# Kernel optimization log

Hardware: AMD Instinct MI355X
Metric: run time of the kernel (lower is better)

## Reference

```python
import jax, jax.numpy as jnp
import numpy as np


def _safe_div(w, n):
    # tf.math.divide_no_nan: returns 0 where denominator is 0
    n = n[:, None]
    return jnp.where(n > 0, w / jnp.where(n > 0, n, 1.0), 0.0)


def setup_inputs() -> dict:
    key = jax.random.key(0)
    x = jax.random.normal(key, (16, 32768, 256), dtype=jnp.float32)
    return {"x": x}


def reference(x):
    # x: [n_models, n_samples, dim]
    n_models = x.shape[0]
    xt = jnp.transpose(x, (1, 0, 2))  # [ns, nm, dim]
    v0 = xt[:, 0, :]
    basis_list = [_safe_div(v0, jnp.linalg.norm(v0, axis=1))]  # each [ns, dim]
    for i in range(1, n_models):
        B = jnp.stack(basis_list, axis=1)              # [ns, i, dim]
        v = xt[:, i, :]                                # [ns, dim]
        coef = jnp.einsum('nd,nid->ni', v, B)          # projections onto basis
        w = v - jnp.einsum('ni,nid->nd', coef, B)      # classical Gram-Schmidt step
        basis_list.append(_safe_div(w, jnp.linalg.norm(w, axis=1)))
    return jnp.stack(basis_list, axis=0)               # [n_models, ns, dim]
```

## Files before the change

kernel.cpp:

```cpp
#include <hip/hip_runtime.h>


constexpr int NM = 16;
constexpr int NR = 32768;
constexpr int D4 = 64;

template <int CTRL, int RMASK>
__device__ __forceinline__ float dpp_add(float x) {
    int xi = __builtin_bit_cast(int, x);
    int yi = __builtin_amdgcn_update_dpp(0, xi, CTRL, RMASK, 0xF, false);
    return x + __builtin_bit_cast(float, yi);
}

__device__ __forceinline__ float wave_sum64(float x) {
    x = dpp_add<0xB1,  0xF>(x);
    x = dpp_add<0x4E,  0xF>(x);
    x = dpp_add<0x141, 0xF>(x);
    x = dpp_add<0x140, 0xF>(x);
    x = dpp_add<0x142, 0xA>(x);
    x = dpp_add<0x143, 0xC>(x);
    int s = __builtin_amdgcn_readlane(__builtin_bit_cast(int, x), 63);
    return __builtin_bit_cast(float, s);
}

__device__ __forceinline__ float dot4(const float4& a, const float4& b) {
    return a.x * b.x + a.y * b.y + a.z * b.z + a.w * b.w;
}

__device__ __forceinline__ void axpy_sub(float4& y, float a, const float4& x) {
    y.x -= a * x.x; y.y -= a * x.y; y.z -= a * x.z; y.w -= a * x.w;
}

__global__ __launch_bounds__(64) void gs_kernel(const float* __restrict__ x,
                                                float* __restrict__ out) {
    const int lane = threadIdx.x;
    const int row  = blockIdx.x;

    const float4* __restrict__ xi = reinterpret_cast<const float4*>(x);
    float4* __restrict__ oo       = reinterpret_cast<float4*>(out);

    float4 v[NM];
#pragma unroll
    for (int i = 0; i < NM; ++i) {
        v[i] = xi[(size_t)(i * NR + row) * D4 + lane];
    }

    auto finalize = [&](int i) {
        float s   = wave_sum64(dot4(v[i], v[i]));
        float inv = rsqrtf(s);
        inv = (s > 0.0f) ? inv : 0.0f;
        v[i].x *= inv; v[i].y *= inv; v[i].z *= inv; v[i].w *= inv;
        oo[(size_t)(i * NR + row) * D4 + lane] = v[i];
    };

    finalize(0);
#pragma unroll
    for (int i = 1; i < 4; ++i) {
        float c[3];
#pragma unroll
        for (int k = 0; k < i; ++k) c[k] = wave_sum64(dot4(v[i], v[k]));
#pragma unroll
        for (int k = 0; k < i; ++k) axpy_sub(v[i], c[k], v[k]);
        finalize(i);
    }

#pragma unroll
    for (int b = 1; b < 4; ++b) {
        const int i0 = 4 * b;
#pragma unroll
        for (int ii = 0; ii < 4; ++ii) {
            float c[12];
#pragma unroll
            for (int k = 0; k < i0; ++k) c[k] = wave_sum64(dot4(v[i0 + ii], v[k]));
#pragma unroll
            for (int k = 0; k < i0; ++k) axpy_sub(v[i0 + ii], c[k], v[k]);
        }
        finalize(i0);
#pragma unroll
        for (int ii = 1; ii < 4; ++ii) {
            float c[3];
#pragma unroll
            for (int k = 0; k < ii; ++k)
                c[k] = wave_sum64(dot4(v[i0 + ii], v[i0 + k]));
#pragma unroll
            for (int k = 0; k < ii; ++k) axpy_sub(v[i0 + ii], c[k], v[i0 + k]);
            finalize(i0 + ii);
        }
    }
}

extern "C" void kernel_launch(void* const* d_in, const int* in_sizes, int n_in,
                              void* d_out, int out_size, void* d_ws, size_t ws_size,
                              hipStream_t stream) {
    const float* x = (const float*)d_in[0];
    float* out     = (float*)d_out;
    dim3 grid(NR);
    dim3 block(64);
    hipLaunchKernelGGL(gs_kernel, grid, block, 0, stream, x, out);
}
```

Before: 219.4 us.

## Process two rows per wave and revert to plain sequential Gram-Schmidt

Each 64-lane wave now handles two sample rows and interleaves their independent dot-product reductions and updates, to expose instruction-level parallelism across the serial DPP reduction chains. The grid is halved to match. The block-wise projection scheme is replaced by straightforward classical Gram-Schmidt against all previous vectors. Register use doubles to about 128 float4 values per lane, which lowers occupancy and may cause spills.

```diff
diff --git a/kernel.cpp b/kernel.cpp
--- a/kernel.cpp
+++ b/kernel.cpp
@@ -1,9 +1,10 @@
 #include <hip/hip_runtime.h>
 
 
-constexpr int NM = 16;
-constexpr int NR = 32768;
-constexpr int D4 = 64;
+constexpr int NM  = 16;
+constexpr int NR  = 32768;
+constexpr int D4  = 64;
+constexpr int RPW = 2;
 
 template <int CTRL, int RMASK>
 __device__ __forceinline__ float dpp_add(float x) {
@@ -34,58 +35,52 @@
 __global__ __launch_bounds__(64) void gs_kernel(const float* __restrict__ x,
                                                 float* __restrict__ out) {
     const int lane = threadIdx.x;
-    const int row  = blockIdx.x;
+    const int r0   = blockIdx.x * RPW;
 
     const float4* __restrict__ xi = reinterpret_cast<const float4*>(x);
     float4* __restrict__ oo       = reinterpret_cast<float4*>(out);
 
-    float4 v[NM];
+    float4 v[RPW][NM];
 #pragma unroll
     for (int i = 0; i < NM; ++i) {
-        v[i] = xi[(size_t)(i * NR + row) * D4 + lane];
+#pragma unroll
+        for (int r = 0; r < RPW; ++r) {
+            v[r][i] = xi[(size_t)(i * NR + r0 + r) * D4 + lane];
+        }
     }
 
     auto finalize = [&](int i) {
-        float s   = wave_sum64(dot4(v[i], v[i]));
-        float inv = rsqrtf(s);
-        inv = (s > 0.0f) ? inv : 0.0f;
-        v[i].x *= inv; v[i].y *= inv; v[i].z *= inv; v[i].w *= inv;
-        oo[(size_t)(i * NR + row) * D4 + lane] = v[i];
+        float s[RPW];
+#pragma unroll
+        for (int r = 0; r < RPW; ++r) s[r] = wave_sum64(dot4(v[r][i], v[r][i]));
+#pragma unroll
+        for (int r = 0; r < RPW; ++r) {
+            float inv = (s[r] > 0.0f) ? rsqrtf(s[r]) : 0.0f;
+            v[r][i].x *= inv; v[r][i].y *= inv; v[r][i].z *= inv; v[r][i].w *= inv;
+            oo[(size_t)(i * NR + r0 + r) * D4 + lane] = v[r][i];
+        }
     };
 
     finalize(0);
-#pragma unroll
-    for (int i = 1; i < 4; ++i) {
-        float c[3];
-#pragma unroll
-        for (int k = 0; k < i; ++k) c[k] = wave_sum64(dot4(v[i], v[k]));
-#pragma unroll
-        for (int k = 0; k < i; ++k) axpy_sub(v[i], c[k], v[k]);
-        finalize(i);
-    }
 
 #pragma unroll
-    for (int b = 1; b < 4; ++b) {
-        const int i0 = 4 * b;
+    for (int i = 1; i < NM; ++i) {
+        float c[RPW][NM - 1];
 #pragma unroll
-        for (int ii = 0; ii < 4; ++ii) {
-            float c[12];
+        for (int k = 0; k < i; ++k) {
 #pragma unroll
-            for (int k = 0; k < i0; ++k) c[k] = wave_sum64(dot4(v[i0 + ii], v[k]));
+            for (int r = 0; r < RPW; ++r) {
+                c[r][k] = wave_sum64(dot4(v[r][i], v[r][k]));
+            }
+        }
 #pragma unroll
-            for (int k = 0; k < i0; ++k) axpy_sub(v[i0 + ii], c[k], v[k]);
+        for (int k = 0; k < i; ++k) {
+#pragma unroll
+            for (int r = 0; r < RPW; ++r) {
+                axpy_sub(v[r][i], c[r][k], v[r][k]);
+            }
         }
-        finalize(i0);
-#pragma unroll
-        for (int ii = 1; ii < 4; ++ii) {
-            float c[3];
-#pragma unroll
-            for (int k = 0; k < ii; ++k)
-                c[k] = wave_sum64(dot4(v[i0 + ii], v[i0 + k]));
-#pragma unroll
-            for (int k = 0; k < ii; ++k) axpy_sub(v[i0 + ii], c[k], v[i0 + k]);
-            finalize(i0 + ii);
-        }
+        finalize(i);
     }
 }
 
@@ -94,7 +89,7 @@
                               hipStream_t stream) {
     const float* x = (const float*)d_in[0];
     float* out     = (float*)d_out;
-    dim3 grid(NR);
+    dim3 grid(NR / RPW);
     dim3 block(64);
     hipLaunchKernelGGL(gs_kernel, grid, block, 0, stream, x, out);
 }
```

Measured after the change: 231.8 us. 1.06x slower.
